# Optimization experiments

Measured on AMD Instinct MI355X. Metric: run time of the kernel, lower is better.

Reference implementation:

```python
import jax, jax.numpy as jnp
import numpy as np

OBS, ACT, EMB, DET, STO = 512, 32, 1024, 1024, 256
T, B = 64, 256
KL_SCALE = 1.0


def setup_inputs() -> dict:
    key = jax.random.key(0)
    ks = jax.random.split(key, 24)
    s = 0.02
    inp = {
        "obs": jax.random.normal(ks[0], (T, B, OBS), jnp.float32),
        "actions": jax.random.normal(ks[1], (T, B, ACT), jnp.float32),
        "rewards": jax.random.normal(ks[2], (T, B), jnp.float32),
        "dones": jnp.zeros((T, B), jnp.bool_),
        "eps": jax.random.normal(ks[3], (T - 1, B, STO), jnp.float32),
        # encoder: Linear(OBS,EMB) -> ReLU -> Linear(EMB,EMB) -> ReLU
        "enc_w1": jax.random.normal(ks[4], (OBS, EMB)) * s,
        "enc_b1": jnp.zeros((EMB,)),
        "enc_w2": jax.random.normal(ks[5], (EMB, EMB)) * s,
        "enc_b2": jnp.zeros((EMB,)),
        # GRUCell(STO+ACT, DET), torch layout [3*DET, in], gate order r,z,n
        "gru_wih": jax.random.normal(ks[6], (3 * DET, STO + ACT)) * s,
        "gru_whh": jax.random.normal(ks[7], (3 * DET, DET)) * s,
        "gru_bih": jnp.zeros((3 * DET,)),
        "gru_bhh": jnp.zeros((3 * DET,)),
        # prior / posterior nets
        "prior_w": jax.random.normal(ks[8], (DET, 2 * STO)) * s,
        "prior_b": jnp.zeros((2 * STO,)),
        "post_w": jax.random.normal(ks[9], (DET + EMB, 2 * STO)) * s,
        "post_b": jnp.zeros((2 * STO,)),
        # obs decoder
        "dec_w1": jax.random.normal(ks[10], (DET + STO, EMB)) * s,
        "dec_b1": jnp.zeros((EMB,)),
        "dec_w2": jax.random.normal(ks[11], (EMB, OBS)) * s,
        "dec_b2": jnp.zeros((OBS,)),
        # reward head
        "rew_w1": jax.random.normal(ks[12], (DET + STO, EMB)) * s,
        "rew_b1": jnp.zeros((EMB,)),
        "rew_w2": jax.random.normal(ks[13], (EMB, 1)) * s,
        "rew_b2": jnp.zeros((1,)),
    }
    return inp


def _kl(mq, lq, mp, lp):
    vq = jnp.exp(2.0 * lq)
    vp = jnp.exp(2.0 * lp)
    kl = lp - lq + (vq + (mq - mp) ** 2) / (vp + 1e-8) - 1.0
    return 0.5 * jnp.sum(kl, axis=-1)


def reference(obs, actions, rewards, dones, eps,
              enc_w1, enc_b1, enc_w2, enc_b2,
              gru_wih, gru_whh, gru_bih, gru_bhh,
              prior_w, prior_b, post_w, post_b,
              dec_w1, dec_b1, dec_w2, dec_b2,
              rew_w1, rew_b1, rew_w2, rew_b2):
    def step(carry, xs):
        h, z = carry
        o_t, o_next, a_t, r_t, d_t, e_t = xs
        # encoder
        emb = jax.nn.relu(jax.nn.relu(o_t @ enc_w1 + enc_b1) @ enc_w2 + enc_b2)
        # prior / posterior
        pm, pl = jnp.split(h @ prior_w + prior_b, 2, axis=-1)
        qm, ql = jnp.split(jnp.concatenate([h, emb], -1) @ post_w + post_b, 2, axis=-1)
        z_post = qm + e_t * jnp.exp(ql)
        # GRUCell (torch semantics)
        x = jnp.concatenate([z_post, a_t], -1)
        gi = x @ gru_wih.T + gru_bih
        gh = h @ gru_whh.T + gru_bhh
        ir, iz, inn = jnp.split(gi, 3, -1)
        hr, hz, hn = jnp.split(gh, 3, -1)
        r = jax.nn.sigmoid(ir + hr)
        u = jax.nn.sigmoid(iz + hz)
        n = jnp.tanh(inn + r * hn)
        h_next = (1.0 - u) * n + u * h
        feat = jnp.concatenate([h_next, z_post], -1)
        pred_obs = jax.nn.relu(feat @ dec_w1 + dec_b1) @ dec_w2 + dec_b2
        pred_rew = (jax.nn.relu(feat @ rew_w1 + rew_b1) @ rew_w2 + rew_b2)[..., 0]
        recon = jnp.mean((pred_obs - o_next) ** 2, axis=-1)  # [B]
        rew_l = (pred_rew - r_t) ** 2                         # [B]
        kl = _kl(qm, ql, pm, pl)                              # [B]
        mask = 1.0 - d_t.astype(h_next.dtype)[:, None]
        return (h_next * mask, z_post * mask), (recon, rew_l, kl)

    h0 = jnp.zeros((B, DET), obs.dtype)
    z0 = jnp.zeros((B, STO), obs.dtype)
    xs = (obs[:-1], obs[1:], actions[:-1], rewards[:-1], dones[:-1], eps)
    _, (recon, rew_l, kl) = jax.lax.scan(step, (h0, z0), xs)
    recon_loss = jnp.mean(recon)
    reward_loss = jnp.mean(rew_l)
    kl_loss = jnp.mean(kl)
    total = recon_loss + reward_loss + KL_SCALE * kl_loss
    return jnp.stack([total, recon_loss, reward_loss, kl_loss])
```

## Files before the change

### kernel.cpp

```cpp
#include <hip/hip_runtime.h>
#include <math.h>


namespace {

typedef unsigned short ushort;
typedef __attribute__((ext_vector_type(8))) short short8;
typedef __attribute__((ext_vector_type(4))) float f32x4;

constexpr int TSTEPS = 63;
constexpr int NB     = 256;
constexpr int NACT   = 32;
constexpr int NROWS  = TSTEPS * NB;
constexpr int TGRP   = 7;
constexpr int NGRP   = 9;
constexpr int GROWS  = TGRP * NB;

constexpr size_t OFF_POSTE = 0;
constexpr size_t OFF_OBSB  = OFF_POSTE + (size_t)NROWS * 512;
constexpr size_t OFF_E1C   = OFF_OBSB + (size_t)GROWS * 512 / 2;
constexpr size_t OFF_EMBC  = OFF_E1C + (size_t)GROWS * 1024 / 2;
constexpr size_t OFF_FEATC = OFF_EMBC + (size_t)GROWS * 1024 / 2;
constexpr size_t OFF_DR1C  = OFF_FEATC + (size_t)GROWS * 1280 / 2;
constexpr size_t OFF_WHT   = OFF_DR1C + (size_t)GROWS * 2048 / 2;
constexpr size_t OFF_WIHT  = OFF_WHT + (size_t)4096 * 1024 / 2;
constexpr size_t OFF_WDRT  = OFF_WIHT + (size_t)3072 * 288 / 2;
constexpr size_t OFF_E1T   = OFF_WDRT + (size_t)2048 * 1280 / 2;
constexpr size_t OFF_E2T   = OFF_E1T + (size_t)1024 * 512 / 2;
constexpr size_t OFF_PET   = OFF_E2T + (size_t)1024 * 1024 / 2;
constexpr size_t OFF_DW2T  = OFF_PET + (size_t)512 * 1024 / 2;
constexpr size_t OFF_BDR   = OFF_DW2T + (size_t)512 * 1024 / 2;
constexpr size_t OFF_G     = OFF_BDR + 2048;
constexpr size_t OFF_H     = OFF_G + (size_t)NB * 3072;
constexpr size_t OFF_HB    = OFF_H + (size_t)NB * 1024;
constexpr size_t OFF_ACC   = OFF_HB + (size_t)NB * 1024 / 2;
constexpr size_t OFF_XBUF  = OFF_ACC + 16;

__device__ __forceinline__ ushort f2bf(float f) {
  unsigned int u = __float_as_uint(f);
  unsigned int r = (u + 0x7fffu + ((u >> 16) & 1u)) >> 16;
  return (ushort)r;
}
__device__ __forceinline__ float bf2f(ushort u) {
  return __uint_as_float((unsigned int)u << 16);
}

__global__ void zero_kernel(float* p, int n) {
  int i = blockIdx.x * 256 + threadIdx.x;
  if (i < n) p[i] = 0.f;
}

__global__ void f2bf_kernel(const float* __restrict__ in, ushort* __restrict__ out, int n) {
  int i = blockIdx.x * 256 + threadIdx.x;
  if (i < n) out[i] = f2bf(in[i]);
}

__global__ void build_wht(const float* __restrict__ prior_w, const float* __restrict__ post_w,
                          const float* __restrict__ whh, ushort* __restrict__ out) {
  int idx = blockIdx.x * 256 + threadIdx.x;
  int n = idx >> 10, k = idx & 1023;
  float v;
  if (n < 1024) {
    int q = (n >> 4) & 3;
    int s = ((n >> 6) << 4) | (n & 15);
    v = (q == 0) ? prior_w[k * 512 + s]
      : (q == 1) ? prior_w[k * 512 + 256 + s]
      : (q == 2) ? post_w[k * 512 + s]
                 : post_w[k * 512 + 256 + s];
  } else {
    v = whh[(size_t)(n - 1024) * 1024 + k];
  }
  out[idx] = f2bf(v);
}

__global__ void trans_conv(const float* __restrict__ in, ushort* __restrict__ out,
                           int ldi, int ldo) {
  __shared__ float tile[32][33];
  int r0 = blockIdx.y * 32, c0 = blockIdx.x * 32;
  int tx = threadIdx.x & 31, ty = threadIdx.x >> 5;
#pragma unroll
  for (int p = 0; p < 4; ++p)
    tile[ty + p * 8][tx] = in[(size_t)(r0 + ty + p * 8) * ldi + c0 + tx];
  __syncthreads();
#pragma unroll
  for (int p = 0; p < 4; ++p)
    out[(size_t)(c0 + ty + p * 8) * ldo + r0 + tx] = f2bf(tile[tx][ty + p * 8]);
}

__global__ void build_bdr(const float* __restrict__ dec_b1, const float* __restrict__ rew_b1,
                          float* __restrict__ bdr) {
  int i = blockIdx.x * 256 + threadIdx.x;
  bdr[i] = (i < 1024) ? dec_b1[i] : rew_b1[i - 1024];
}

template <int EPI, bool AF32>
__global__ __launch_bounds__(256) void gemm_bf16(
    const void* __restrict__ Av, const ushort* __restrict__ BT,
    const float* __restrict__ bias, void* __restrict__ Cv,
    int K, int lda, int ldb, int ldc) {
  __shared__ __align__(16) ushort As[2][64 * 40];
  __shared__ __align__(16) ushort Bs[2][64 * 40];
  int tid = threadIdx.x;
  int wave = tid >> 6, lane = tid & 63;
  int quad = lane >> 4, l15 = lane & 15;
  int m0 = blockIdx.y * 64, n0 = blockIdx.x * 64;
  int sr = tid >> 2, sc = (tid & 3) * 8;
  const ushort* agb = (const ushort*)Av + (size_t)(m0 + sr) * lda + sc;
  const float*  agf = (const float*)Av + (size_t)(m0 + sr) * lda + sc;
  const ushort* bgp = BT + (size_t)(n0 + sr) * ldb + sc;
  int4 pa0, pa1, pb;
  if (AF32) { pa0 = *(const int4*)agf; pa1 = *(const int4*)(agf + 4); }
  else      { pa0 = *(const int4*)agb; }
  pb = *(const int4*)bgp;
  f32x4 acc[4] = {};
  int buf = 0;
  for (int k0 = 0; k0 < K; k0 += 32, buf ^= 1) {
    int4 st;
    if (AF32) {
      float f[8];
      *(int4*)&f[0] = pa0; *(int4*)&f[4] = pa1;
      ushort u[8];
#pragma unroll
      for (int i = 0; i < 8; ++i) u[i] = f2bf(f[i]);
      st = *(const int4*)u;
    } else {
      st = pa0;
    }
    *(int4*)&As[buf][sr * 40 + sc] = st;
    *(int4*)&Bs[buf][sr * 40 + sc] = pb;
    __syncthreads();
    int kn = k0 + 32;
    if (kn < K) {
      if (AF32) { pa0 = *(const int4*)(agf + kn); pa1 = *(const int4*)(agf + kn + 4); }
      else      { pa0 = *(const int4*)(agb + kn); }
      pb = *(const int4*)(bgp + kn);
    }
    short8 a = *(const short8*)&As[buf][(wave * 16 + l15) * 40 + quad * 8];
#pragma unroll
    for (int c = 0; c < 4; ++c) {
      short8 b = *(const short8*)&Bs[buf][(c * 16 + l15) * 40 + quad * 8];
      acc[c] = __builtin_amdgcn_mfma_f32_16x16x32_bf16(a, b, acc[c], 0, 0, 0);
    }
  }
#pragma unroll
  for (int c = 0; c < 4; ++c) {
#pragma unroll
    for (int r = 0; r < 4; ++r) {
      size_t row = m0 + wave * 16 + quad * 4 + r;
      int col = n0 + c * 16 + l15;
      float v = acc[c][r] + bias[col];
      if (EPI == 1) v = fmaxf(v, 0.f);
      if (EPI == 1) ((ushort*)Cv)[row * ldc + col] = f2bf(v);
      else ((float*)Cv)[row * ldc + col] = v;
    }
  }
}

__global__ __launch_bounds__(256) void step_g_kernel(
    int t, int tt, const ushort* __restrict__ HB, const ushort* __restrict__ WHT,
    const float* __restrict__ prior_b, const float* __restrict__ poste,
    const float* __restrict__ eps, const float* __restrict__ actions,
    float* __restrict__ G, ushort* __restrict__ xbuf,
    ushort* __restrict__ featc, float* __restrict__ acc_kl) {
  __shared__ __align__(16) ushort As[2][64 * 72];
  __shared__ __align__(16) ushort Bs[2][64 * 72];
  int tid = threadIdx.x;
  int wave = tid >> 6, lane = tid & 63;
  int quad = lane >> 4, l15 = lane & 15;
  int m0 = blockIdx.y * 64, n0 = blockIdx.x * 64;
  int sr = tid >> 2, sc = (tid & 3) * 16;
  const ushort* agp = HB + (size_t)(m0 + sr) * 1024 + sc;
  const ushort* bgp = WHT + (size_t)(n0 + sr) * 1024 + sc;
  int4 a0 = *(const int4*)agp, a1 = *(const int4*)(agp + 8);
  int4 b0 = *(const int4*)bgp, b1 = *(const int4*)(bgp + 8);
  f32x4 acc[4] = {};
  int buf = 0;
  for (int k0 = 0; k0 < 1024; k0 += 64, buf ^= 1) {
    *(int4*)&As[buf][sr * 72 + sc] = a0; *(int4*)&As[buf][sr * 72 + sc + 8] = a1;
    *(int4*)&Bs[buf][sr * 72 + sc] = b0; *(int4*)&Bs[buf][sr * 72 + sc + 8] = b1;
    __syncthreads();
    int kn = k0 + 64;
    if (kn < 1024) {
      a0 = *(const int4*)(agp + kn); a1 = *(const int4*)(agp + kn + 8);
      b0 = *(const int4*)(bgp + kn); b1 = *(const int4*)(bgp + kn + 8);
    }
#pragma unroll
    for (int kk = 0; kk < 2; ++kk) {
      short8 a = *(const short8*)&As[buf][(wave * 16 + l15) * 72 + kk * 32 + quad * 8];
#pragma unroll
      for (int c = 0; c < 4; ++c) {
        short8 b = *(const short8*)&Bs[buf][(c * 16 + l15) * 72 + kk * 32 + quad * 8];
        acc[c] = __builtin_amdgcn_mfma_f32_16x16x32_bf16(a, b, acc[c], 0, 0, 0);
      }
    }
  }
  if (blockIdx.x < 16) {
    int s = (n0 >> 2) + l15;
    float kl_sum = 0.f;
#pragma unroll
    for (int r = 0; r < 4; ++r) {
      int b = m0 + wave * 16 + quad * 4 + r;
      size_t row = (size_t)t * NB + b;
      float pm = acc[0][r] + prior_b[s];
      float pl = acc[1][r] + prior_b[256 + s];
      float qm = acc[2][r] + poste[row * 512 + s];
      float ql = acc[3][r] + poste[row * 512 + 256 + s];
      float e = eps[row * 256 + s];
      float z = qm + e * expf(ql);
      xbuf[b * 288 + s] = f2bf(z);
      featc[(size_t)(tt * NB + b) * 1280 + 1024 + s] = f2bf(z);
      if (s < NACT) xbuf[b * 288 + 256 + s] = f2bf(actions[row * NACT + s]);
      float vq = expf(2.f * ql), vp = expf(2.f * pl);
      float dm = qm - pm;
      kl_sum += pl - ql + (vq + dm * dm) / (vp + 1e-8f) - 1.f;
    }
    for (int off = 32; off > 0; off >>= 1) kl_sum += __shfl_down(kl_sum, off);
    if (lane == 0) atomicAdd(acc_kl, 0.5f * kl_sum);
  } else {
    int ng = n0 - 1024;
#pragma unroll
    for (int c = 0; c < 4; ++c)
#pragma unroll
      for (int r = 0; r < 4; ++r) {
        int b = m0 + wave * 16 + quad * 4 + r;
        G[(size_t)b * 3072 + ng + c * 16 + l15] = acc[c][r];
      }
  }
}

__global__ __launch_bounds__(128) void gru_step_kernel(
    int t, int tt, const ushort* __restrict__ xbuf, const ushort* __restrict__ wiht,
    const float* __restrict__ G, const float* __restrict__ bih,
    const float* __restrict__ bhh, const unsigned char* __restrict__ dones,
    float* __restrict__ H, ushort* __restrict__ HB, ushort* __restrict__ featc) {
  __shared__ __align__(16) ushort As[2][32 * 40];
  __shared__ __align__(16) ushort Bs[2][3][64 * 40];
  int tid = threadIdx.x;
  int wave = tid >> 6, lane = tid & 63;
  int quad = lane >> 4, l15 = lane & 15;
  int m0 = blockIdx.y * 32, n0 = blockIdx.x * 64;
  int ar = tid >> 2, ac = (tid & 3) * 8;
  int br = tid >> 1, bc = (tid & 1) * 16;
  const ushort* agp = xbuf + (size_t)(m0 + ar) * 288 + ac;
  const ushort* bgp = wiht + (size_t)(n0 + br) * 288 + bc;
  int4 pa = *(const int4*)agp;
  int4 pb[3][2];
#pragma unroll
  for (int gg = 0; gg < 3; ++gg) {
    pb[gg][0] = *(const int4*)(bgp + (size_t)gg * 1024 * 288);
    pb[gg][1] = *(const int4*)(bgp + (size_t)gg * 1024 * 288 + 8);
  }
  f32x4 accv[3][4] = {};
  int buf = 0;
  for (int k0 = 0; k0 < 288; k0 += 32, buf ^= 1) {
    *(int4*)&As[buf][ar * 40 + ac] = pa;
#pragma unroll
    for (int gg = 0; gg < 3; ++gg) {
      *(int4*)&Bs[buf][gg][br * 40 + bc] = pb[gg][0];
      *(int4*)&Bs[buf][gg][br * 40 + bc + 8] = pb[gg][1];
    }
    __syncthreads();
    int kn = k0 + 32;
    if (kn < 288) {
      pa = *(const int4*)(agp + kn);
#pragma unroll
      for (int gg = 0; gg < 3; ++gg) {
        pb[gg][0] = *(const int4*)(bgp + (size_t)gg * 1024 * 288 + kn);
        pb[gg][1] = *(const int4*)(bgp + (size_t)gg * 1024 * 288 + kn + 8);
      }
    }
    short8 a = *(const short8*)&As[buf][(wave * 16 + l15) * 40 + quad * 8];
#pragma unroll
    for (int gg = 0; gg < 3; ++gg) {
#pragma unroll
      for (int c = 0; c < 4; ++c) {
        short8 b = *(const short8*)&Bs[buf][gg][(c * 16 + l15) * 40 + quad * 8];
        accv[gg][c] = __builtin_amdgcn_mfma_f32_16x16x32_bf16(a, b, accv[gg][c], 0, 0, 0);
      }
    }
  }
#pragma unroll
  for (int c = 0; c < 4; ++c) {
#pragma unroll
    for (int r = 0; r < 4; ++r) {
      int b_idx = m0 + wave * 16 + quad * 4 + r;
      int j = n0 + c * 16 + l15;
      const float* g = G + (size_t)b_idx * 3072;
      float ir = accv[0][c][r] + bih[j];
      float iz = accv[1][c][r] + bih[1024 + j];
      float in_ = accv[2][c][r] + bih[2048 + j];
      float hr = g[j] + bhh[j];
      float hz = g[1024 + j] + bhh[1024 + j];
      float hn = g[2048 + j] + bhh[2048 + j];
      float rg = 1.f / (1.f + expf(-(ir + hr)));
      float u = 1.f / (1.f + expf(-(iz + hz)));
      float n = tanhf(in_ + rg * hn);
      float hprev = H[b_idx * 1024 + j];
      float hnext = (1.f - u) * n + u * hprev;
      featc[(size_t)(tt * NB + b_idx) * 1280 + j] = f2bf(hnext);
      float mask = 1.f - (float)dones[t * NB + b_idx];
      float hm = hnext * mask;
      H[b_idx * 1024 + j] = hm;
      HB[b_idx * 1024 + j] = f2bf(hm);
    }
  }
}

__global__ __launch_bounds__(256) void decobs_loss_kernel(
    const ushort* __restrict__ A, const ushort* __restrict__ BT,
    const float* __restrict__ bias, const float* __restrict__ obs_next_g,
    float* __restrict__ acc) {
  __shared__ __align__(16) ushort As[2][64 * 40];
  __shared__ __align__(16) ushort Bs[2][64 * 40];
  int tid = threadIdx.x;
  int wave = tid >> 6, lane = tid & 63;
  int quad = lane >> 4, l15 = lane & 15;
  int m0 = blockIdx.y * 64, n0 = blockIdx.x * 64;
  int sr = tid >> 2, sc = (tid & 3) * 8;
  const ushort* agp = A + (size_t)(m0 + sr) * 2048 + sc;
  const ushort* bgp = BT + (size_t)(n0 + sr) * 1024 + sc;
  int4 pa = *(const int4*)agp;
  int4 pb = *(const int4*)bgp;
  f32x4 accm[4] = {};
  int buf = 0;
  for (int k0 = 0; k0 < 1024; k0 += 32, buf ^= 1) {
    *(int4*)&As[buf][sr * 40 + sc] = pa;
    *(int4*)&Bs[buf][sr * 40 + sc] = pb;
    __syncthreads();
    int kn = k0 + 32;
    if (kn < 1024) {
      pa = *(const int4*)(agp + kn);
      pb = *(const int4*)(bgp + kn);
    }
    short8 a = *(const short8*)&As[buf][(wave * 16 + l15) * 40 + quad * 8];
#pragma unroll
    for (int c = 0; c < 4; ++c) {
      short8 b = *(const short8*)&Bs[buf][(c * 16 + l15) * 40 + quad * 8];
      accm[c] = __builtin_amdgcn_mfma_f32_16x16x32_bf16(a, b, accm[c], 0, 0, 0);
    }
  }
  float local = 0.f;
#pragma unroll
  for (int c = 0; c < 4; ++c) {
#pragma unroll
    for (int r = 0; r < 4; ++r) {
      size_t row = m0 + wave * 16 + quad * 4 + r;
      int col = n0 + c * 16 + l15;
      float v = accm[c][r] + bias[col];
      float d = v - obs_next_g[row * 512 + col];
      local += d * d;
    }
  }
  __shared__ float red[256];
  red[tid] = local;
  __syncthreads();
  for (int st = 128; st > 0; st >>= 1) {
    if (tid < st) red[tid] += red[tid + st];
    __syncthreads();
  }
  if (tid == 0) atomicAdd(&acc[0], red[0]);
}

__global__ __launch_bounds__(256) void rew_loss_kernel(
    const ushort* __restrict__ R1, const float* __restrict__ w2,
    const float* __restrict__ b2, const float* __restrict__ rewards_g,
    float* __restrict__ acc) {
  int wave = threadIdx.x >> 6;
  int lane = threadIdx.x & 63;
  int row = blockIdx.x * 4 + wave;
  const ushort* rp = R1 + (size_t)row * 2048;
  float s = 0.f;
#pragma unroll
  for (int i = 0; i < 16; ++i) s += bf2f(rp[lane + 64 * i]) * w2[lane + 64 * i];
  for (int off = 32; off > 0; off >>= 1) s += __shfl_down(s, off);
  if (lane == 0) {
    float d = s + b2[0] - rewards_g[row];
    atomicAdd(&acc[1], d * d);
  }
}

__global__ void finalize_kernel(const float* __restrict__ acc, float* __restrict__ out) {
  float recon = acc[0] / ((float)NROWS * 512.f);
  float rew = acc[1] / (float)NROWS;
  float kl = acc[2] / (float)NROWS;
  out[0] = recon + rew + kl;
  out[1] = recon;
  out[2] = rew;
  out[3] = kl;
}

}

extern "C" void kernel_launch(void* const* d_in, const int* in_sizes, int n_in,
                              void* d_out, int out_size, void* d_ws, size_t ws_size,
                              hipStream_t stream) {
  const float* obs     = (const float*)d_in[0];
  const float* actions = (const float*)d_in[1];
  const float* rewards = (const float*)d_in[2];
  const unsigned char* dones = (const unsigned char*)d_in[3];
  const float* eps     = (const float*)d_in[4];
  const float* enc_w1  = (const float*)d_in[5];
  const float* enc_b1  = (const float*)d_in[6];
  const float* enc_w2  = (const float*)d_in[7];
  const float* enc_b2  = (const float*)d_in[8];
  const float* gru_wih = (const float*)d_in[9];
  const float* gru_whh = (const float*)d_in[10];
  const float* gru_bih = (const float*)d_in[11];
  const float* gru_bhh = (const float*)d_in[12];
  const float* prior_w = (const float*)d_in[13];
  const float* prior_b = (const float*)d_in[14];
  const float* post_w  = (const float*)d_in[15];
  const float* post_b  = (const float*)d_in[16];
  const float* dec_w1  = (const float*)d_in[17];
  const float* dec_b1  = (const float*)d_in[18];
  const float* dec_w2  = (const float*)d_in[19];
  const float* dec_b2  = (const float*)d_in[20];
  const float* rew_w1  = (const float*)d_in[21];
  const float* rew_b1  = (const float*)d_in[22];
  const float* rew_w2  = (const float*)d_in[23];
  const float* rew_b2  = (const float*)d_in[24];
  float* out = (float*)d_out;
  float* ws = (float*)d_ws;

  float*  POSTE = ws + OFF_POSTE;
  ushort* E1C   = (ushort*)(ws + OFF_E1C);
  ushort* EMBC  = (ushort*)(ws + OFF_EMBC);
  ushort* FEATC = (ushort*)(ws + OFF_FEATC);
  ushort* DR1C  = (ushort*)(ws + OFF_DR1C);
  ushort* WHT   = (ushort*)(ws + OFF_WHT);
  ushort* WIHT  = (ushort*)(ws + OFF_WIHT);
  ushort* WDRT  = (ushort*)(ws + OFF_WDRT);
  ushort* E1T   = (ushort*)(ws + OFF_E1T);
  ushort* E2T   = (ushort*)(ws + OFF_E2T);
  ushort* PET   = (ushort*)(ws + OFF_PET);
  ushort* DW2T  = (ushort*)(ws + OFF_DW2T);
  float*  BDR   = ws + OFF_BDR;
  float*  G     = ws + OFF_G;
  float*  H     = ws + OFF_H;
  ushort* HB    = (ushort*)(ws + OFF_HB);
  float*  ACC   = ws + OFF_ACC;
  ushort* XBUF  = (ushort*)(ws + OFF_XBUF);

  {
    int nzero = NB * 1024 + NB * 512 + 16;
    zero_kernel<<<(nzero + 255) / 256, 256, 0, stream>>>(H, nzero);
  }
  build_wht<<<4096 * 1024 / 256, 256, 0, stream>>>(prior_w, post_w, gru_whh, WHT);
  f2bf_kernel<<<(3072 * 288) / 256, 256, 0, stream>>>(gru_wih, WIHT, 3072 * 288);
  trans_conv<<<dim3(1024 / 32, 1280 / 32), 256, 0, stream>>>(dec_w1, WDRT, 1024, 1280);
  trans_conv<<<dim3(1024 / 32, 1280 / 32), 256, 0, stream>>>(rew_w1, WDRT + (size_t)1024 * 1280, 1024, 1280);
  trans_conv<<<dim3(1024 / 32, 512 / 32), 256, 0, stream>>>(enc_w1, E1T, 1024, 512);
  trans_conv<<<dim3(1024 / 32, 1024 / 32), 256, 0, stream>>>(enc_w2, E2T, 1024, 1024);
  trans_conv<<<dim3(512 / 32, 1024 / 32), 256, 0, stream>>>(post_w + (size_t)1024 * 512, PET, 512, 1024);
  trans_conv<<<dim3(512 / 32, 1024 / 32), 256, 0, stream>>>(dec_w2, DW2T, 512, 1024);
  build_bdr<<<8, 256, 0, stream>>>(dec_b1, rew_b1, BDR);

  for (int g = 0; g < NGRP; ++g) {
    const float* obs_g = obs + (size_t)g * GROWS * 512;
    gemm_bf16<1, true><<<dim3(16, GROWS / 64), 256, 0, stream>>>(
        (const void*)obs_g, E1T, enc_b1, E1C, 512, 512, 512, 1024);
    gemm_bf16<1, false><<<dim3(16, GROWS / 64), 256, 0, stream>>>(
        (const void*)E1C, E2T, enc_b2, EMBC, 1024, 1024, 1024, 1024);
    gemm_bf16<2, false><<<dim3(8, GROWS / 64), 256, 0, stream>>>(
        (const void*)EMBC, PET, post_b, POSTE + (size_t)g * GROWS * 512, 1024, 1024, 1024, 512);
  }

  for (int g = 0; g < NGRP; ++g) {
    for (int tt = 0; tt < TGRP; ++tt) {
      int t = g * TGRP + tt;
      step_g_kernel<<<dim3(64, 4), 256, 0, stream>>>(
          t, tt, HB, WHT, prior_b, POSTE, eps, actions, G, XBUF, FEATC, &ACC[2]);
      gru_step_kernel<<<dim3(16, 8), 128, 0, stream>>>(
          t, tt, XBUF, WIHT, G, gru_bih, gru_bhh, dones, H, HB, FEATC);
    }
    gemm_bf16<1, false><<<dim3(32, GROWS / 64), 256, 0, stream>>>(
        (const void*)FEATC, WDRT, BDR, DR1C, 1280, 1280, 1280, 2048);
    decobs_loss_kernel<<<dim3(8, GROWS / 64), 256, 0, stream>>>(
        DR1C, DW2T, dec_b2, obs + ((size_t)g * TGRP + 1) * NB * 512, ACC);
    rew_loss_kernel<<<GROWS / 4, 256, 0, stream>>>(
        DR1C + 1024, rew_w2, rew_b2, rewards + (size_t)g * TGRP * NB, ACC);
  }

  finalize_kernel<<<1, 1, 0, stream>>>(ACC, out);
}
```

Baseline: 3.044 ms.

## Fuse per-timestep recurrent kernels into one cooperative kernel per time group

Replaces the two kernel launches per timestep (hidden-state GEMM with prior/posterior sampling and KL, then the GRU input GEMM and gate update) with one cooperative kernel per group of 7 timesteps. Grid-wide syncs separate the phases instead of kernel boundaries. This removes about 14 launches per group and their launch gaps on the sequential recurrence, at the cost of grid.sync overhead and a fixed 256-block grid. If the cooperative launch fails, the code falls back to the old per-step launches.

```diff
diff --git a/kernel.cpp b/kernel.cpp
--- a/kernel.cpp
+++ b/kernel.cpp
@@ -1,6 +1,9 @@
 #include <hip/hip_runtime.h>
+#include <hip/hip_cooperative_groups.h>
 #include <math.h>
 
+
+namespace cg = cooperative_groups;
 
 namespace {
 
@@ -153,6 +156,171 @@
       if (EPI == 1) ((ushort*)Cv)[row * ldc + col] = f2bf(v);
       else ((float*)Cv)[row * ldc + col] = v;
     }
+  }
+}
+
+__global__ __launch_bounds__(256) void phaseb_group_kernel(
+    int g0,
+    ushort* __restrict__ HB, const ushort* __restrict__ WHT,
+    const float* __restrict__ prior_b, const float* __restrict__ poste,
+    const float* __restrict__ eps, const float* __restrict__ actions,
+    const unsigned char* __restrict__ dones,
+    const ushort* __restrict__ wiht, const float* __restrict__ bih,
+    const float* __restrict__ bhh,
+    float* __restrict__ G, ushort* __restrict__ xbuf,
+    float* __restrict__ H, ushort* __restrict__ featc,
+    float* __restrict__ acc_kl) {
+  __shared__ __align__(16) char smem[36864];
+  ushort* As1 = (ushort*)smem;
+  ushort* Bs1 = (ushort*)(smem + 18432);
+  ushort* As2 = (ushort*)smem;
+  ushort* Bs2 = (ushort*)(smem + 5120);
+  cg::grid_group grid = cg::this_grid();
+
+  int tid = threadIdx.x;
+  int wave = tid >> 6, lane = tid & 63;
+  int quad = lane >> 4, l15 = lane & 15;
+  int bid = blockIdx.x;
+
+  int bx1 = bid & 63, by1 = bid >> 6;
+  int m01 = by1 * 64, n01 = bx1 * 64;
+  int sr1 = tid >> 2, sc1 = (tid & 3) * 16;
+  const ushort* agp1 = HB + (size_t)(m01 + sr1) * 1024 + sc1;
+  const ushort* bgp1 = WHT + (size_t)(n01 + sr1) * 1024 + sc1;
+
+  int bx2 = bid & 15, by2 = bid >> 4;
+  int m02 = by2 * 32, n02 = bx2 * 64;
+  int ar2 = tid >> 2, ac2 = (tid & 3) * 8;
+  int br2 = tid >> 2, bc2 = (tid & 3) * 8;
+  const ushort* agp2 = xbuf + (size_t)(m02 + ar2) * 288 + ac2;
+  const ushort* bgp2 = wiht + (size_t)(n02 + br2) * 288 + bc2;
+
+  for (int tt = 0; tt < TGRP; ++tt) {
+    int t = g0 + tt;
+    {
+      int4 a0 = *(const int4*)agp1, a1 = *(const int4*)(agp1 + 8);
+      int4 b0 = *(const int4*)bgp1, b1 = *(const int4*)(bgp1 + 8);
+      f32x4 acc[4] = {};
+      int buf = 0;
+      for (int k0 = 0; k0 < 1024; k0 += 64, buf ^= 1) {
+        ushort* as = As1 + buf * 4608;
+        ushort* bs = Bs1 + buf * 4608;
+        *(int4*)&as[sr1 * 72 + sc1] = a0; *(int4*)&as[sr1 * 72 + sc1 + 8] = a1;
+        *(int4*)&bs[sr1 * 72 + sc1] = b0; *(int4*)&bs[sr1 * 72 + sc1 + 8] = b1;
+        __syncthreads();
+        int kn = k0 + 64;
+        if (kn < 1024) {
+          a0 = *(const int4*)(agp1 + kn); a1 = *(const int4*)(agp1 + kn + 8);
+          b0 = *(const int4*)(bgp1 + kn); b1 = *(const int4*)(bgp1 + kn + 8);
+        }
+#pragma unroll
+        for (int kk = 0; kk < 2; ++kk) {
+          short8 a = *(const short8*)&as[(wave * 16 + l15) * 72 + kk * 32 + quad * 8];
+#pragma unroll
+          for (int c = 0; c < 4; ++c) {
+            short8 b = *(const short8*)&bs[(c * 16 + l15) * 72 + kk * 32 + quad * 8];
+            acc[c] = __builtin_amdgcn_mfma_f32_16x16x32_bf16(a, b, acc[c], 0, 0, 0);
+          }
+        }
+        if (kn < 1024) __syncthreads();
+      }
+      if (bx1 < 16) {
+        int s = (n01 >> 2) + l15;
+        float kl_sum = 0.f;
+#pragma unroll
+        for (int r = 0; r < 4; ++r) {
+          int b = m01 + wave * 16 + quad * 4 + r;
+          size_t row = (size_t)t * NB + b;
+          float pm = acc[0][r] + prior_b[s];
+          float pl = acc[1][r] + prior_b[256 + s];
+          float qm = acc[2][r] + poste[row * 512 + s];
+          float ql = acc[3][r] + poste[row * 512 + 256 + s];
+          float e = eps[row * 256 + s];
+          float z = qm + e * expf(ql);
+          xbuf[b * 288 + s] = f2bf(z);
+          featc[(size_t)(tt * NB + b) * 1280 + 1024 + s] = f2bf(z);
+          if (s < NACT) xbuf[b * 288 + 256 + s] = f2bf(actions[row * NACT + s]);
+          float vq = expf(2.f * ql), vp = expf(2.f * pl);
+          float dm = qm - pm;
+          kl_sum += pl - ql + (vq + dm * dm) / (vp + 1e-8f) - 1.f;
+        }
+        for (int off = 32; off > 0; off >>= 1) kl_sum += __shfl_down(kl_sum, off);
+        if (lane == 0) atomicAdd(acc_kl, 0.5f * kl_sum);
+      } else {
+        int ng = n01 - 1024;
+#pragma unroll
+        for (int c = 0; c < 4; ++c)
+#pragma unroll
+          for (int r = 0; r < 4; ++r) {
+            int b = m01 + wave * 16 + quad * 4 + r;
+            G[(size_t)b * 3072 + ng + c * 16 + l15] = acc[c][r];
+          }
+      }
+    }
+    __threadfence();
+    grid.sync();
+    if (bid < 128) {
+      int4 pa = {};
+      if (tid < 128) pa = *(const int4*)agp2;
+      int4 pb0 = *(const int4*)bgp2;
+      int4 pb1 = *(const int4*)(bgp2 + (size_t)1024 * 288);
+      int4 pb2 = *(const int4*)(bgp2 + (size_t)2048 * 288);
+      f32x4 accv[3][2] = {};
+      int buf = 0;
+      for (int k0 = 0; k0 < 288; k0 += 32, buf ^= 1) {
+        ushort* as = As2 + buf * 1280;
+        ushort* bs = Bs2 + buf * 7680;
+        if (tid < 128) *(int4*)&as[ar2 * 40 + ac2] = pa;
+        *(int4*)&bs[br2 * 40 + bc2] = pb0;
+        *(int4*)&bs[2560 + br2 * 40 + bc2] = pb1;
+        *(int4*)&bs[5120 + br2 * 40 + bc2] = pb2;
+        __syncthreads();
+        int kn = k0 + 32;
+        if (kn < 288) {
+          if (tid < 128) pa = *(const int4*)(agp2 + kn);
+          pb0 = *(const int4*)(bgp2 + kn);
+          pb1 = *(const int4*)(bgp2 + (size_t)1024 * 288 + kn);
+          pb2 = *(const int4*)(bgp2 + (size_t)2048 * 288 + kn);
+        }
+        short8 a = *(const short8*)&as[((wave & 1) * 16 + l15) * 40 + quad * 8];
+#pragma unroll
+        for (int gg = 0; gg < 3; ++gg) {
+#pragma unroll
+          for (int c = 0; c < 2; ++c) {
+            short8 b = *(const short8*)&bs[gg * 2560 + ((wave >> 1) * 32 + c * 16 + l15) * 40 + quad * 8];
+            accv[gg][c] = __builtin_amdgcn_mfma_f32_16x16x32_bf16(a, b, accv[gg][c], 0, 0, 0);
+          }
+        }
+        if (kn < 288) __syncthreads();
+      }
+#pragma unroll
+      for (int c = 0; c < 2; ++c) {
+#pragma unroll
+        for (int r = 0; r < 4; ++r) {
+          int b_idx = m02 + (wave & 1) * 16 + quad * 4 + r;
+          int j = n02 + (wave >> 1) * 32 + c * 16 + l15;
+          const float* g = G + (size_t)b_idx * 3072;
+          float ir = accv[0][c][r] + bih[j];
+          float iz = accv[1][c][r] + bih[1024 + j];
+          float in_ = accv[2][c][r] + bih[2048 + j];
+          float hr = g[j] + bhh[j];
+          float hz = g[1024 + j] + bhh[1024 + j];
+          float hn = g[2048 + j] + bhh[2048 + j];
+          float rg = 1.f / (1.f + expf(-(ir + hr)));
+          float u = 1.f / (1.f + expf(-(iz + hz)));
+          float n = tanhf(in_ + rg * hn);
+          float hprev = H[b_idx * 1024 + j];
+          float hnext = (1.f - u) * n + u * hprev;
+          featc[(size_t)(tt * NB + b_idx) * 1280 + j] = f2bf(hnext);
+          float mask = 1.f - (float)dones[t * NB + b_idx];
+          float hm = hnext * mask;
+          H[b_idx * 1024 + j] = hm;
+          HB[b_idx * 1024 + j] = f2bf(hm);
+        }
+      }
+    }
+    __threadfence();
+    grid.sync();
   }
 }
 
@@ -465,13 +633,28 @@
         (const void*)EMBC, PET, post_b, POSTE + (size_t)g * GROWS * 512, 1024, 1024, 1024, 512);
   }
 
+  float* acckl = ACC + 2;
+  int coop_ok = 1;
   for (int g = 0; g < NGRP; ++g) {
-    for (int tt = 0; tt < TGRP; ++tt) {
-      int t = g * TGRP + tt;
-      step_g_kernel<<<dim3(64, 4), 256, 0, stream>>>(
-          t, tt, HB, WHT, prior_b, POSTE, eps, actions, G, XBUF, FEATC, &ACC[2]);
-      gru_step_kernel<<<dim3(16, 8), 128, 0, stream>>>(
-          t, tt, XBUF, WIHT, G, gru_bih, gru_bhh, dones, H, HB, FEATC);
+    int g0 = g * TGRP;
+    if (coop_ok) {
+      void* kargs[] = {
+          (void*)&g0, (void*)&HB, (void*)&WHT, (void*)&prior_b, (void*)&POSTE,
+          (void*)&eps, (void*)&actions, (void*)&dones, (void*)&WIHT,
+          (void*)&gru_bih, (void*)&gru_bhh, (void*)&G, (void*)&XBUF,
+          (void*)&H, (void*)&FEATC, (void*)&acckl};
+      hipError_t ce = hipLaunchCooperativeKernel(
+          (const void*)phaseb_group_kernel, dim3(256), dim3(256), kargs, 0, stream);
+      if (ce != hipSuccess) coop_ok = 0;
+    }
+    if (!coop_ok) {
+      for (int tt = 0; tt < TGRP; ++tt) {
+        int t = g0 + tt;
+        step_g_kernel<<<dim3(64, 4), 256, 0, stream>>>(
+            t, tt, HB, WHT, prior_b, POSTE, eps, actions, G, XBUF, FEATC, acckl);
+        gru_step_kernel<<<dim3(16, 8), 128, 0, stream>>>(
+            t, tt, XBUF, WIHT, G, gru_bih, gru_bhh, dones, H, HB, FEATC);
+      }
     }
     gemm_bf16<1, false><<<dim3(32, GROWS / 64), 256, 0, stream>>>(
         (const void*)FEATC, WDRT, BDR, DR1C, 1280, 1280, 1280, 2048);
```

Result: slower. 9.597 ms (+215.3%).

## Fuse per-timestep recurrent kernels into persistent group kernel with flag sync

Applied to the files above, without the earlier changes.

Replaces the two kernel launches per timestep (recurrent GEMM plus prior/posterior epilogue, and the GRU input GEMM plus gate update) with one persistent kernel per group of 7 timesteps. Blocks sync through monotonically increasing per-row-tile atomic counters in workspace instead of kernel boundaries. The goal is to remove launch overhead and the idle gaps between the many small dependent launches on the serial recurrence. In exchange it assumes all 256 blocks are resident at once, uses spin-waits with fences, and moves the GRU stage to 64 blocks with 64-row tiles.

```diff
diff --git a/kernel.cpp b/kernel.cpp
--- a/kernel.cpp
+++ b/kernel.cpp
@@ -35,6 +35,7 @@
 constexpr size_t OFF_HB    = OFF_H + (size_t)NB * 1024;
 constexpr size_t OFF_ACC   = OFF_HB + (size_t)NB * 1024 / 2;
 constexpr size_t OFF_XBUF  = OFF_ACC + 16;
+constexpr size_t OFF_FLAGS = OFF_XBUF + (size_t)NB * 288 / 2;
 
 __device__ __forceinline__ ushort f2bf(float f) {
   unsigned int u = __float_as_uint(f);
@@ -156,152 +157,177 @@
   }
 }
 
-__global__ __launch_bounds__(256) void step_g_kernel(
-    int t, int tt, const ushort* __restrict__ HB, const ushort* __restrict__ WHT,
+__global__ __launch_bounds__(256) void phaseb_group_kernel(
+    int g0,
+    ushort* __restrict__ HB, const ushort* __restrict__ WHT,
     const float* __restrict__ prior_b, const float* __restrict__ poste,
     const float* __restrict__ eps, const float* __restrict__ actions,
+    const unsigned char* __restrict__ dones,
+    const ushort* __restrict__ wiht, const float* __restrict__ bih,
+    const float* __restrict__ bhh,
     float* __restrict__ G, ushort* __restrict__ xbuf,
-    ushort* __restrict__ featc, float* __restrict__ acc_kl) {
-  __shared__ __align__(16) ushort As[2][64 * 72];
-  __shared__ __align__(16) ushort Bs[2][64 * 72];
+    float* __restrict__ H, ushort* __restrict__ featc,
+    float* __restrict__ acc_kl, int* __restrict__ flags) {
+  __shared__ __align__(16) char smem[40960];
+  ushort* As1 = (ushort*)smem;
+  ushort* Bs1 = (ushort*)(smem + 18432);
+  ushort* As2 = (ushort*)smem;
+  ushort* Bs2 = (ushort*)(smem + 10240);
+  int* flagA = flags;
+  int* flagB = flags + 4;
+
   int tid = threadIdx.x;
   int wave = tid >> 6, lane = tid & 63;
   int quad = lane >> 4, l15 = lane & 15;
-  int m0 = blockIdx.y * 64, n0 = blockIdx.x * 64;
-  int sr = tid >> 2, sc = (tid & 3) * 16;
-  const ushort* agp = HB + (size_t)(m0 + sr) * 1024 + sc;
-  const ushort* bgp = WHT + (size_t)(n0 + sr) * 1024 + sc;
-  int4 a0 = *(const int4*)agp, a1 = *(const int4*)(agp + 8);
-  int4 b0 = *(const int4*)bgp, b1 = *(const int4*)(bgp + 8);
-  f32x4 acc[4] = {};
-  int buf = 0;
-  for (int k0 = 0; k0 < 1024; k0 += 64, buf ^= 1) {
-    *(int4*)&As[buf][sr * 72 + sc] = a0; *(int4*)&As[buf][sr * 72 + sc + 8] = a1;
-    *(int4*)&Bs[buf][sr * 72 + sc] = b0; *(int4*)&Bs[buf][sr * 72 + sc + 8] = b1;
+  int bid = blockIdx.x;
+  int n1 = bid & 63, m = bid >> 6;
+  int m0 = m * 64, n01 = n1 * 64;
+
+  int sr1 = tid >> 2, sc1 = (tid & 3) * 16;
+  const ushort* agp1 = HB + (size_t)(m0 + sr1) * 1024 + sc1;
+  const ushort* bgp1 = WHT + (size_t)(n01 + sr1) * 1024 + sc1;
+  int sr2 = tid >> 2, sc2 = (tid & 3) * 8;
+  const ushort* agp2 = xbuf + (size_t)(m0 + sr2) * 288 + sc2;
+  const ushort* bgp2 = wiht + (size_t)(n01 + sr2) * 288 + sc2;
+
+  for (int tt = 0; tt < TGRP; ++tt) {
+    int t = g0 + tt;
+    if (tid == 0) {
+      while (__hip_atomic_load(&flagB[m], __ATOMIC_ACQUIRE, __HIP_MEMORY_SCOPE_AGENT) < 16 * t)
+        __builtin_amdgcn_s_sleep(1);
+    }
     __syncthreads();
-    int kn = k0 + 64;
-    if (kn < 1024) {
-      a0 = *(const int4*)(agp + kn); a1 = *(const int4*)(agp + kn + 8);
-      b0 = *(const int4*)(bgp + kn); b1 = *(const int4*)(bgp + kn + 8);
-    }
-#pragma unroll
-    for (int kk = 0; kk < 2; ++kk) {
-      short8 a = *(const short8*)&As[buf][(wave * 16 + l15) * 72 + kk * 32 + quad * 8];
+    {
+      int4 a0 = *(const int4*)agp1, a1 = *(const int4*)(agp1 + 8);
+      int4 b0 = *(const int4*)bgp1, b1 = *(const int4*)(bgp1 + 8);
+      f32x4 acc[4] = {};
+      int buf = 0;
+      for (int k0 = 0; k0 < 1024; k0 += 64, buf ^= 1) {
+        ushort* as = As1 + buf * 4608;
+        ushort* bs = Bs1 + buf * 4608;
+        *(int4*)&as[sr1 * 72 + sc1] = a0; *(int4*)&as[sr1 * 72 + sc1 + 8] = a1;
+        *(int4*)&bs[sr1 * 72 + sc1] = b0; *(int4*)&bs[sr1 * 72 + sc1 + 8] = b1;
+        __syncthreads();
+        int kn = k0 + 64;
+        if (kn < 1024) {
+          a0 = *(const int4*)(agp1 + kn); a1 = *(const int4*)(agp1 + kn + 8);
+          b0 = *(const int4*)(bgp1 + kn); b1 = *(const int4*)(bgp1 + kn + 8);
+        }
+#pragma unroll
+        for (int kk = 0; kk < 2; ++kk) {
+          short8 a = *(const short8*)&as[(wave * 16 + l15) * 72 + kk * 32 + quad * 8];
+#pragma unroll
+          for (int c = 0; c < 4; ++c) {
+            short8 b = *(const short8*)&bs[(c * 16 + l15) * 72 + kk * 32 + quad * 8];
+            acc[c] = __builtin_amdgcn_mfma_f32_16x16x32_bf16(a, b, acc[c], 0, 0, 0);
+          }
+        }
+      }
+      if (n1 < 16) {
+        int s = (n01 >> 2) + l15;
+        float kl_sum = 0.f;
+#pragma unroll
+        for (int r = 0; r < 4; ++r) {
+          int b = m0 + wave * 16 + quad * 4 + r;
+          size_t row = (size_t)t * NB + b;
+          float pm = acc[0][r] + prior_b[s];
+          float pl = acc[1][r] + prior_b[256 + s];
+          float qm = acc[2][r] + poste[row * 512 + s];
+          float ql = acc[3][r] + poste[row * 512 + 256 + s];
+          float e = eps[row * 256 + s];
+          float z = qm + e * expf(ql);
+          xbuf[b * 288 + s] = f2bf(z);
+          featc[(size_t)(tt * NB + b) * 1280 + 1024 + s] = f2bf(z);
+          if (s < NACT) xbuf[b * 288 + 256 + s] = f2bf(actions[row * NACT + s]);
+          float vq = expf(2.f * ql), vp = expf(2.f * pl);
+          float dm = qm - pm;
+          kl_sum += pl - ql + (vq + dm * dm) / (vp + 1e-8f) - 1.f;
+        }
+        for (int off = 32; off > 0; off >>= 1) kl_sum += __shfl_down(kl_sum, off);
+        if (lane == 0) atomicAdd(acc_kl, 0.5f * kl_sum);
+      } else {
+        int ng = n01 - 1024;
+#pragma unroll
+        for (int c = 0; c < 4; ++c)
+#pragma unroll
+          for (int r = 0; r < 4; ++r) {
+            int b = m0 + wave * 16 + quad * 4 + r;
+            G[(size_t)b * 3072 + ng + c * 16 + l15] = acc[c][r];
+          }
+      }
+    }
+    __syncthreads();
+    if (tid == 0) {
+      __threadfence();
+      __hip_atomic_fetch_add(&flagA[m], 1, __ATOMIC_RELAXED, __HIP_MEMORY_SCOPE_AGENT);
+    }
+    if (n1 < 16) {
+      if (tid == 0) {
+        while (__hip_atomic_load(&flagA[m], __ATOMIC_ACQUIRE, __HIP_MEMORY_SCOPE_AGENT) < 64 * (t + 1))
+          __builtin_amdgcn_s_sleep(1);
+      }
+      __syncthreads();
+      int4 pa = *(const int4*)agp2;
+      int4 pb0 = *(const int4*)bgp2;
+      int4 pb1 = *(const int4*)(bgp2 + (size_t)1024 * 288);
+      int4 pb2 = *(const int4*)(bgp2 + (size_t)2048 * 288);
+      f32x4 accv[3][4] = {};
+      int buf = 0;
+      for (int k0 = 0; k0 < 288; k0 += 32, buf ^= 1) {
+        ushort* as = As2 + buf * 2560;
+        ushort* bs = Bs2 + buf * 7680;
+        *(int4*)&as[sr2 * 40 + sc2] = pa;
+        *(int4*)&bs[sr2 * 40 + sc2] = pb0;
+        *(int4*)&bs[2560 + sr2 * 40 + sc2] = pb1;
+        *(int4*)&bs[5120 + sr2 * 40 + sc2] = pb2;
+        __syncthreads();
+        int kn = k0 + 32;
+        if (kn < 288) {
+          pa = *(const int4*)(agp2 + kn);
+          pb0 = *(const int4*)(bgp2 + kn);
+          pb1 = *(const int4*)(bgp2 + (size_t)1024 * 288 + kn);
+          pb2 = *(const int4*)(bgp2 + (size_t)2048 * 288 + kn);
+        }
+        short8 a = *(const short8*)&as[(wave * 16 + l15) * 40 + quad * 8];
+#pragma unroll
+        for (int gg = 0; gg < 3; ++gg) {
+#pragma unroll
+          for (int c = 0; c < 4; ++c) {
+            short8 b = *(const short8*)&bs[gg * 2560 + (c * 16 + l15) * 40 + quad * 8];
+            accv[gg][c] = __builtin_amdgcn_mfma_f32_16x16x32_bf16(a, b, accv[gg][c], 0, 0, 0);
+          }
+        }
+      }
 #pragma unroll
       for (int c = 0; c < 4; ++c) {
-        short8 b = *(const short8*)&Bs[buf][(c * 16 + l15) * 72 + kk * 32 + quad * 8];
-        acc[c] = __builtin_amdgcn_mfma_f32_16x16x32_bf16(a, b, acc[c], 0, 0, 0);
+#pragma unroll
+        for (int r = 0; r < 4; ++r) {
+          int b_idx = m0 + wave * 16 + quad * 4 + r;
+          int j = n01 + c * 16 + l15;
+          const float* g = G + (size_t)b_idx * 3072;
+          float ir = accv[0][c][r] + bih[j];
+          float iz = accv[1][c][r] + bih[1024 + j];
+          float in_ = accv[2][c][r] + bih[2048 + j];
+          float hr = g[j] + bhh[j];
+          float hz = g[1024 + j] + bhh[1024 + j];
+          float hn = g[2048 + j] + bhh[2048 + j];
+          float rg = 1.f / (1.f + expf(-(ir + hr)));
+          float u = 1.f / (1.f + expf(-(iz + hz)));
+          float n = tanhf(in_ + rg * hn);
+          float hprev = H[b_idx * 1024 + j];
+          float hnext = (1.f - u) * n + u * hprev;
+          featc[(size_t)(tt * NB + b_idx) * 1280 + j] = f2bf(hnext);
+          float mask = 1.f - (float)dones[t * NB + b_idx];
+          float hm = hnext * mask;
+          H[b_idx * 1024 + j] = hm;
+          HB[b_idx * 1024 + j] = f2bf(hm);
+        }
       }
-    }
-  }
-  if (blockIdx.x < 16) {
-    int s = (n0 >> 2) + l15;
-    float kl_sum = 0.f;
-#pragma unroll
-    for (int r = 0; r < 4; ++r) {
-      int b = m0 + wave * 16 + quad * 4 + r;
-      size_t row = (size_t)t * NB + b;
-      float pm = acc[0][r] + prior_b[s];
-      float pl = acc[1][r] + prior_b[256 + s];
-      float qm = acc[2][r] + poste[row * 512 + s];
-      float ql = acc[3][r] + poste[row * 512 + 256 + s];
-      float e = eps[row * 256 + s];
-      float z = qm + e * expf(ql);
-      xbuf[b * 288 + s] = f2bf(z);
-      featc[(size_t)(tt * NB + b) * 1280 + 1024 + s] = f2bf(z);
-      if (s < NACT) xbuf[b * 288 + 256 + s] = f2bf(actions[row * NACT + s]);
-      float vq = expf(2.f * ql), vp = expf(2.f * pl);
-      float dm = qm - pm;
-      kl_sum += pl - ql + (vq + dm * dm) / (vp + 1e-8f) - 1.f;
-    }
-    for (int off = 32; off > 0; off >>= 1) kl_sum += __shfl_down(kl_sum, off);
-    if (lane == 0) atomicAdd(acc_kl, 0.5f * kl_sum);
-  } else {
-    int ng = n0 - 1024;
-#pragma unroll
-    for (int c = 0; c < 4; ++c)
-#pragma unroll
-      for (int r = 0; r < 4; ++r) {
-        int b = m0 + wave * 16 + quad * 4 + r;
-        G[(size_t)b * 3072 + ng + c * 16 + l15] = acc[c][r];
+      __syncthreads();
+      if (tid == 0) {
+        __threadfence();
+        __hip_atomic_fetch_add(&flagB[m], 1, __ATOMIC_RELAXED, __HIP_MEMORY_SCOPE_AGENT);
       }
-  }
-}
-
-__global__ __launch_bounds__(128) void gru_step_kernel(
-    int t, int tt, const ushort* __restrict__ xbuf, const ushort* __restrict__ wiht,
-    const float* __restrict__ G, const float* __restrict__ bih,
-    const float* __restrict__ bhh, const unsigned char* __restrict__ dones,
-    float* __restrict__ H, ushort* __restrict__ HB, ushort* __restrict__ featc) {
-  __shared__ __align__(16) ushort As[2][32 * 40];
-  __shared__ __align__(16) ushort Bs[2][3][64 * 40];
-  int tid = threadIdx.x;
-  int wave = tid >> 6, lane = tid & 63;
-  int quad = lane >> 4, l15 = lane & 15;
-  int m0 = blockIdx.y * 32, n0 = blockIdx.x * 64;
-  int ar = tid >> 2, ac = (tid & 3) * 8;
-  int br = tid >> 1, bc = (tid & 1) * 16;
-  const ushort* agp = xbuf + (size_t)(m0 + ar) * 288 + ac;
-  const ushort* bgp = wiht + (size_t)(n0 + br) * 288 + bc;
-  int4 pa = *(const int4*)agp;
-  int4 pb[3][2];
-#pragma unroll
-  for (int gg = 0; gg < 3; ++gg) {
-    pb[gg][0] = *(const int4*)(bgp + (size_t)gg * 1024 * 288);
-    pb[gg][1] = *(const int4*)(bgp + (size_t)gg * 1024 * 288 + 8);
-  }
-  f32x4 accv[3][4] = {};
-  int buf = 0;
-  for (int k0 = 0; k0 < 288; k0 += 32, buf ^= 1) {
-    *(int4*)&As[buf][ar * 40 + ac] = pa;
-#pragma unroll
-    for (int gg = 0; gg < 3; ++gg) {
-      *(int4*)&Bs[buf][gg][br * 40 + bc] = pb[gg][0];
-      *(int4*)&Bs[buf][gg][br * 40 + bc + 8] = pb[gg][1];
-    }
-    __syncthreads();
-    int kn = k0 + 32;
-    if (kn < 288) {
-      pa = *(const int4*)(agp + kn);
-#pragma unroll
-      for (int gg = 0; gg < 3; ++gg) {
-        pb[gg][0] = *(const int4*)(bgp + (size_t)gg * 1024 * 288 + kn);
-        pb[gg][1] = *(const int4*)(bgp + (size_t)gg * 1024 * 288 + kn + 8);
-      }
-    }
-    short8 a = *(const short8*)&As[buf][(wave * 16 + l15) * 40 + quad * 8];
-#pragma unroll
-    for (int gg = 0; gg < 3; ++gg) {
-#pragma unroll
-      for (int c = 0; c < 4; ++c) {
-        short8 b = *(const short8*)&Bs[buf][gg][(c * 16 + l15) * 40 + quad * 8];
-        accv[gg][c] = __builtin_amdgcn_mfma_f32_16x16x32_bf16(a, b, accv[gg][c], 0, 0, 0);
-      }
-    }
-  }
-#pragma unroll
-  for (int c = 0; c < 4; ++c) {
-#pragma unroll
-    for (int r = 0; r < 4; ++r) {
-      int b_idx = m0 + wave * 16 + quad * 4 + r;
-      int j = n0 + c * 16 + l15;
-      const float* g = G + (size_t)b_idx * 3072;
-      float ir = accv[0][c][r] + bih[j];
-      float iz = accv[1][c][r] + bih[1024 + j];
-      float in_ = accv[2][c][r] + bih[2048 + j];
-      float hr = g[j] + bhh[j];
-      float hz = g[1024 + j] + bhh[1024 + j];
-      float hn = g[2048 + j] + bhh[2048 + j];
-      float rg = 1.f / (1.f + expf(-(ir + hr)));
-      float u = 1.f / (1.f + expf(-(iz + hz)));
-      float n = tanhf(in_ + rg * hn);
-      float hprev = H[b_idx * 1024 + j];
-      float hnext = (1.f - u) * n + u * hprev;
-      featc[(size_t)(tt * NB + b_idx) * 1280 + j] = f2bf(hnext);
-      float mask = 1.f - (float)dones[t * NB + b_idx];
-      float hm = hnext * mask;
-      H[b_idx * 1024 + j] = hm;
-      HB[b_idx * 1024 + j] = f2bf(hm);
     }
   }
 }
@@ -440,9 +466,10 @@
   ushort* HB    = (ushort*)(ws + OFF_HB);
   float*  ACC   = ws + OFF_ACC;
   ushort* XBUF  = (ushort*)(ws + OFF_XBUF);
+  int*    FLAGS = (int*)(ws + OFF_FLAGS);
 
   {
-    int nzero = NB * 1024 + NB * 512 + 16;
+    int nzero = NB * 1024 + NB * 512 + 16 + NB * 288 / 2 + 16;
     zero_kernel<<<(nzero + 255) / 256, 256, 0, stream>>>(H, nzero);
   }
   build_wht<<<4096 * 1024 / 256, 256, 0, stream>>>(prior_w, post_w, gru_whh, WHT);
@@ -465,14 +492,12 @@
         (const void*)EMBC, PET, post_b, POSTE + (size_t)g * GROWS * 512, 1024, 1024, 1024, 512);
   }
 
+  float* acckl = ACC + 2;
   for (int g = 0; g < NGRP; ++g) {
-    for (int tt = 0; tt < TGRP; ++tt) {
-      int t = g * TGRP + tt;
-      step_g_kernel<<<dim3(64, 4), 256, 0, stream>>>(
-          t, tt, HB, WHT, prior_b, POSTE, eps, actions, G, XBUF, FEATC, &ACC[2]);
-      gru_step_kernel<<<dim3(16, 8), 128, 0, stream>>>(
-          t, tt, XBUF, WIHT, G, gru_bih, gru_bhh, dones, H, HB, FEATC);
-    }
+    int g0 = g * TGRP;
+    phaseb_group_kernel<<<256, 256, 0, stream>>>(
+        g0, HB, WHT, prior_b, POSTE, eps, actions, dones, WIHT,
+        gru_bih, gru_bhh, G, XBUF, H, FEATC, acckl, FLAGS);
     gemm_bf16<1, false><<<dim3(32, GROWS / 64), 256, 0, stream>>>(
         (const void*)FEATC, WDRT, BDR, DR1C, 1280, 1280, 1280, 2048);
     decobs_loss_kernel<<<dim3(8, GROWS / 64), 256, 0, stream>>>(
```

Measured after the change: 9.744 ms. 3.2x slower.

## Add larger-tile bf16 GEMM for encoder and decoder layers; tile latent weight transpose

Applied to the files above, without the earlier changes.

Adds a gemm_big kernel using 64x128 or 128x128 block tiles, where each wave computes 4xNT MFMA tiles, for more operand reuse per LDS load. It replaces the small-tile GEMM for both encoder layers and the decoder/reward first layer. The prior/posterior weight packing becomes a shared-memory tiled transpose, and the GRU hidden weight conversion becomes a plain f2bf copy, so global reads are coalesced. The trade-off is more registers per thread, which lowers occupancy, and fewer blocks in flight for the small per-group GEMMs.

```diff
diff --git a/kernel.cpp b/kernel.cpp
--- a/kernel.cpp
+++ b/kernel.cpp
@@ -55,22 +55,24 @@
   if (i < n) out[i] = f2bf(in[i]);
 }
 
-__global__ void build_wht(const float* __restrict__ prior_w, const float* __restrict__ post_w,
-                          const float* __restrict__ whh, ushort* __restrict__ out) {
-  int idx = blockIdx.x * 256 + threadIdx.x;
-  int n = idx >> 10, k = idx & 1023;
-  float v;
-  if (n < 1024) {
-    int q = (n >> 4) & 3;
-    int s = ((n >> 6) << 4) | (n & 15);
-    v = (q == 0) ? prior_w[k * 512 + s]
-      : (q == 1) ? prior_w[k * 512 + 256 + s]
-      : (q == 2) ? post_w[k * 512 + s]
-                 : post_w[k * 512 + 256 + s];
-  } else {
-    v = whh[(size_t)(n - 1024) * 1024 + k];
-  }
-  out[idx] = f2bf(v);
+__global__ void build_wht_latent(const float* __restrict__ prior_w,
+                                 const float* __restrict__ post_w,
+                                 ushort* __restrict__ out) {
+  __shared__ float tile[32][33];
+  int k0 = blockIdx.x * 32, n0 = blockIdx.y * 32;
+  int tx = threadIdx.x & 31, ty = threadIdx.x >> 5;
+  int n = n0 + tx;
+  int q = (n >> 4) & 3;
+  int s = ((n >> 6) << 4) | (n & 15);
+  const float* src = (q < 2) ? prior_w : post_w;
+  int col = (q & 1) ? (256 + s) : s;
+#pragma unroll
+  for (int p = 0; p < 4; ++p)
+    tile[ty + p * 8][tx] = src[(size_t)(k0 + ty + p * 8) * 512 + col];
+  __syncthreads();
+#pragma unroll
+  for (int p = 0; p < 4; ++p)
+    out[(size_t)(n0 + ty + p * 8) * 1024 + k0 + tx] = f2bf(tile[tx][ty + p * 8]);
 }
 
 __global__ void trans_conv(const float* __restrict__ in, ushort* __restrict__ out,
@@ -154,6 +156,87 @@
       else ((float*)Cv)[row * ldc + col] = v;
     }
   }
+}
+
+template <int BM, int EPI, bool AF32>
+__global__ __launch_bounds__(256) void gemm_big(
+    const void* __restrict__ Av, const ushort* __restrict__ BT,
+    const float* __restrict__ bias, void* __restrict__ Cv,
+    int K, int lda, int ldb, int ldc) {
+  constexpr int BN = 128;
+  constexpr int WM = BM / 64;
+  constexpr int WN = 4 / WM;
+  constexpr int NT = BN / WN / 16;
+  __shared__ __align__(16) ushort As[2][BM * 40];
+  __shared__ __align__(16) ushort Bs[2][BN * 40];
+  int tid = threadIdx.x;
+  int w = tid >> 6, lane = tid & 63;
+  int quad = lane >> 4, l15 = lane & 15;
+  int wm = (WM == 1) ? 0 : (w >> 1);
+  int wn = (WM == 1) ? w : (w & 1);
+  int m0 = blockIdx.y * BM, n0 = blockIdx.x * BN;
+  int sar = (BM == 64) ? (tid >> 2) : (tid >> 1);
+  int sac = (BM == 64) ? ((tid & 3) * 8) : ((tid & 1) * 16);
+  int sbr = tid >> 1, sbc = (tid & 1) * 16;
+  const ushort* agb = (const ushort*)Av + (size_t)(m0 + sar) * lda + sac;
+  const float*  agf = (const float*)Av + (size_t)(m0 + sar) * lda + sac;
+  const ushort* bgp = BT + (size_t)(n0 + sbr) * ldb + sbc;
+  int4 pa0, pa1, pb0, pb1;
+  if (AF32)         { pa0 = *(const int4*)agf; pa1 = *(const int4*)(agf + 4); }
+  else if (BM == 64){ pa0 = *(const int4*)agb; }
+  else              { pa0 = *(const int4*)agb; pa1 = *(const int4*)(agb + 8); }
+  pb0 = *(const int4*)bgp; pb1 = *(const int4*)(bgp + 8);
+  f32x4 acc[4][NT] = {};
+  int buf = 0;
+  for (int k0 = 0; k0 < K; k0 += 32, buf ^= 1) {
+    if (AF32) {
+      float f[8];
+      *(int4*)&f[0] = pa0; *(int4*)&f[4] = pa1;
+      ushort u[8];
+#pragma unroll
+      for (int i = 0; i < 8; ++i) u[i] = f2bf(f[i]);
+      *(int4*)&As[buf][sar * 40 + sac] = *(const int4*)u;
+    } else if (BM == 64) {
+      *(int4*)&As[buf][sar * 40 + sac] = pa0;
+    } else {
+      *(int4*)&As[buf][sar * 40 + sac] = pa0;
+      *(int4*)&As[buf][sar * 40 + sac + 8] = pa1;
+    }
+    *(int4*)&Bs[buf][sbr * 40 + sbc] = pb0;
+    *(int4*)&Bs[buf][sbr * 40 + sbc + 8] = pb1;
+    __syncthreads();
+    int kn = k0 + 32;
+    if (kn < K) {
+      if (AF32)          { pa0 = *(const int4*)(agf + kn); pa1 = *(const int4*)(agf + kn + 4); }
+      else if (BM == 64) { pa0 = *(const int4*)(agb + kn); }
+      else               { pa0 = *(const int4*)(agb + kn); pa1 = *(const int4*)(agb + kn + 8); }
+      pb0 = *(const int4*)(bgp + kn); pb1 = *(const int4*)(bgp + kn + 8);
+    }
+    short8 af[4], bfr[NT];
+#pragma unroll
+    for (int mt = 0; mt < 4; ++mt)
+      af[mt] = *(const short8*)&As[buf][(wm * 64 + mt * 16 + l15) * 40 + quad * 8];
+#pragma unroll
+    for (int nt = 0; nt < NT; ++nt)
+      bfr[nt] = *(const short8*)&Bs[buf][(wn * (BN / WN) + nt * 16 + l15) * 40 + quad * 8];
+#pragma unroll
+    for (int mt = 0; mt < 4; ++mt)
+#pragma unroll
+      for (int nt = 0; nt < NT; ++nt)
+        acc[mt][nt] = __builtin_amdgcn_mfma_f32_16x16x32_bf16(af[mt], bfr[nt], acc[mt][nt], 0, 0, 0);
+  }
+#pragma unroll
+  for (int mt = 0; mt < 4; ++mt)
+#pragma unroll
+    for (int nt = 0; nt < NT; ++nt)
+#pragma unroll
+      for (int r = 0; r < 4; ++r) {
+        size_t row = m0 + wm * 64 + mt * 16 + quad * 4 + r;
+        int col = n0 + wn * (BN / WN) + nt * 16 + l15;
+        float v = acc[mt][nt][r] + bias[col];
+        if (EPI == 1) { v = fmaxf(v, 0.f); ((ushort*)Cv)[row * ldc + col] = f2bf(v); }
+        else ((float*)Cv)[row * ldc + col] = v;
+      }
 }
 
 __global__ __launch_bounds__(256) void step_g_kernel(
@@ -445,7 +528,9 @@
     int nzero = NB * 1024 + NB * 512 + 16;
     zero_kernel<<<(nzero + 255) / 256, 256, 0, stream>>>(H, nzero);
   }
-  build_wht<<<4096 * 1024 / 256, 256, 0, stream>>>(prior_w, post_w, gru_whh, WHT);
+  build_wht_latent<<<dim3(32, 32), 256, 0, stream>>>(prior_w, post_w, WHT);
+  f2bf_kernel<<<(3072 * 1024) / 256, 256, 0, stream>>>(
+      gru_whh, WHT + (size_t)1024 * 1024, 3072 * 1024);
   f2bf_kernel<<<(3072 * 288) / 256, 256, 0, stream>>>(gru_wih, WIHT, 3072 * 288);
   trans_conv<<<dim3(1024 / 32, 1280 / 32), 256, 0, stream>>>(dec_w1, WDRT, 1024, 1280);
   trans_conv<<<dim3(1024 / 32, 1280 / 32), 256, 0, stream>>>(rew_w1, WDRT + (size_t)1024 * 1280, 1024, 1280);
@@ -457,23 +542,24 @@
 
   for (int g = 0; g < NGRP; ++g) {
     const float* obs_g = obs + (size_t)g * GROWS * 512;
-    gemm_bf16<1, true><<<dim3(16, GROWS / 64), 256, 0, stream>>>(
+    gemm_big<64, 1, true><<<dim3(1024 / 128, GROWS / 64), 256, 0, stream>>>(
         (const void*)obs_g, E1T, enc_b1, E1C, 512, 512, 512, 1024);
-    gemm_bf16<1, false><<<dim3(16, GROWS / 64), 256, 0, stream>>>(
+    gemm_big<64, 1, false><<<dim3(1024 / 128, GROWS / 64), 256, 0, stream>>>(
         (const void*)E1C, E2T, enc_b2, EMBC, 1024, 1024, 1024, 1024);
     gemm_bf16<2, false><<<dim3(8, GROWS / 64), 256, 0, stream>>>(
         (const void*)EMBC, PET, post_b, POSTE + (size_t)g * GROWS * 512, 1024, 1024, 1024, 512);
   }
 
+  float* acckl = ACC + 2;
   for (int g = 0; g < NGRP; ++g) {
     for (int tt = 0; tt < TGRP; ++tt) {
       int t = g * TGRP + tt;
       step_g_kernel<<<dim3(64, 4), 256, 0, stream>>>(
-          t, tt, HB, WHT, prior_b, POSTE, eps, actions, G, XBUF, FEATC, &ACC[2]);
+          t, tt, HB, WHT, prior_b, POSTE, eps, actions, G, XBUF, FEATC, acckl);
       gru_step_kernel<<<dim3(16, 8), 128, 0, stream>>>(
           t, tt, XBUF, WIHT, G, gru_bih, gru_bhh, dones, H, HB, FEATC);
     }
-    gemm_bf16<1, false><<<dim3(32, GROWS / 64), 256, 0, stream>>>(
+    gemm_big<128, 1, false><<<dim3(2048 / 128, GROWS / 128), 256, 0, stream>>>(
         (const void*)FEATC, WDRT, BDR, DR1C, 1280, 1280, 1280, 2048);
     decobs_loss_kernel<<<dim3(8, GROWS / 64), 256, 0, stream>>>(
         DR1C, DW2T, dec_b2, obs + ((size_t)g * TGRP + 1) * NB * 512, ACC);
```

Measured after the change: 3.056 ms. Within noise of the previous version (+0.4%).
